# Kernel tuning notes

Hardware: AMD Instinct MI355X
Metric: run time of the kernel (lower is better)

Reference implementation:

```python
import jax, jax.numpy as jnp
import numpy as np

TOTAL = 262144
FEAT = 512
NSEG = 1024


def setup_inputs() -> dict:
    key = jax.random.key(0)
    k1, k2 = jax.random.split(key)
    batch = jax.random.normal(k1, (TOTAL, FEAT), dtype=jnp.float32)
    segment_ids = jnp.sort(jax.random.randint(k2, (TOTAL,), 0, NSEG)).astype(jnp.int32)
    return {"batch": batch, "segment_ids": segment_ids, "num_segments": NSEG}


def reference(batch, segment_ids, num_segments):
    # mode='mean', keep_shape=True: per-segment mean, broadcast back to rows.
    seg_sum = jax.ops.segment_sum(batch, segment_ids, num_segments=num_segments)
    counts = jax.ops.segment_sum(
        jnp.ones((batch.shape[0],), dtype=batch.dtype), segment_ids,
        num_segments=num_segments)
    means = seg_sum / jnp.maximum(counts, 1.0)[:, None]  # [NSEG, FEAT]
    out = jnp.take(means, segment_ids, axis=0)           # keep_shape expand
    return out
```

## Files before the change

### kernel.cpp

```cpp
#include <hip/hip_runtime.h>

#define FEAT 512
#define F4   128
#define NSEG 1024
#define CHUNK 256

typedef float f4_t __attribute__((ext_vector_type(4)));

__global__ void bounds_zero_kernel(const int* __restrict__ seg,
                                   int* __restrict__ starts,
                                   float* __restrict__ sums, int total) {
    int i = blockIdx.x * blockDim.x + threadIdx.x;
    if (sums != nullptr && i < NSEG * FEAT / 2) {
        ((float2*)sums)[i] = make_float2(0.f, 0.f);
    }
    if (i >= total) return;
    int cur = seg[i];
    int prev = (i == 0) ? -1 : seg[i - 1];
    for (int s = prev + 1; s <= cur; ++s) starts[s] = i;
    if (i == total - 1) {
        for (int s = cur + 1; s <= NSEG; ++s) starts[s] = total;
    }
}

__global__ __launch_bounds__(512) void chunk_sum_kernel(
        const float* __restrict__ batch,
        const int* __restrict__ seg,
        const int* __restrict__ starts,
        float* __restrict__ sums, int total) {
    const int tid  = threadIdx.x;
    const int lane = tid & (F4 - 1);
    const int rg   = tid >> 7;
    const int r0   = blockIdx.x * CHUNK;
    if (r0 >= total) return;
    const int r1   = min(r0 + CHUNK, total);

    const int s0 = seg[r0];
    const int s1 = seg[r1 - 1];

    const f4_t* b4 = (const f4_t*)batch;
    __shared__ f4_t red[4][F4];

    for (int s = s0; s <= s1; ++s) {
        const int a = max(starts[s], r0);
        const int b = min(starts[s + 1], r1);
        if (a >= b) continue;

        f4_t a0 = (f4_t)(0.f);
        f4_t a1 = (f4_t)(0.f);
        int r = a + rg;
        for (; r + 28 < b; r += 32) {
            const f4_t* p = b4 + (size_t)r * F4 + lane;
            f4_t v0 = __builtin_nontemporal_load(p + 0 * 4 * F4);
            f4_t v1 = __builtin_nontemporal_load(p + 1 * 4 * F4);
            f4_t v2 = __builtin_nontemporal_load(p + 2 * 4 * F4);
            f4_t v3 = __builtin_nontemporal_load(p + 3 * 4 * F4);
            f4_t v4 = __builtin_nontemporal_load(p + 4 * 4 * F4);
            f4_t v5 = __builtin_nontemporal_load(p + 5 * 4 * F4);
            f4_t v6 = __builtin_nontemporal_load(p + 6 * 4 * F4);
            f4_t v7 = __builtin_nontemporal_load(p + 7 * 4 * F4);
            a0 += v0; a1 += v1;
            a0 += v2; a1 += v3;
            a0 += v4; a1 += v5;
            a0 += v6; a1 += v7;
        }
        for (; r < b; r += 4) {
            a0 += __builtin_nontemporal_load(b4 + (size_t)r * F4 + lane);
        }
        a0 += a1;

        red[rg][lane] = a0;
        __syncthreads();
        if (rg == 0) {
            f4_t t = red[0][lane] + red[1][lane] + red[2][lane] + red[3][lane];
            float* dst = sums + (size_t)s * FEAT + lane * 4;
            atomicAdd(dst + 0, t.x);
            atomicAdd(dst + 1, t.y);
            atomicAdd(dst + 2, t.z);
            atomicAdd(dst + 3, t.w);
        }
        __syncthreads();
    }
}

__global__ __launch_bounds__(256) void broadcast_chunk_kernel(
        const int* __restrict__ seg,
        const int* __restrict__ starts,
        const float* __restrict__ sums,
        float* __restrict__ out, int total) {
    const int tid  = threadIdx.x;
    const int lane = tid & (F4 - 1);
    const int rg   = tid >> 7;
    const int r0   = blockIdx.x * CHUNK;
    if (r0 >= total) return;
    const int r1   = min(r0 + CHUNK, total);

    const int s0 = seg[r0];
    const int s1 = seg[r1 - 1];

    const f4_t* m4 = (const f4_t*)sums;
    f4_t* o4 = (f4_t*)out;

    for (int s = s0; s <= s1; ++s) {
        const int sa = starts[s];
        const int sb = starts[s + 1];
        const int a = max(sa, r0);
        const int b = min(sb, r1);
        if (a >= b) continue;
        const int count = sb - sa;
        const float inv = 1.0f / (float)(count > 0 ? count : 1);
        const f4_t mean = m4[(size_t)s * F4 + lane] * inv;
        int r = a + rg;
        for (; r + 14 < b; r += 16) {
            f4_t* q = o4 + (size_t)r * F4 + lane;
            __builtin_nontemporal_store(mean, q + 0 * 2 * F4);
            __builtin_nontemporal_store(mean, q + 1 * 2 * F4);
            __builtin_nontemporal_store(mean, q + 2 * 2 * F4);
            __builtin_nontemporal_store(mean, q + 3 * 2 * F4);
            __builtin_nontemporal_store(mean, q + 4 * 2 * F4);
            __builtin_nontemporal_store(mean, q + 5 * 2 * F4);
            __builtin_nontemporal_store(mean, q + 6 * 2 * F4);
            __builtin_nontemporal_store(mean, q + 7 * 2 * F4);
        }
        for (; r < b; r += 2) {
            __builtin_nontemporal_store(mean, o4 + (size_t)r * F4 + lane);
        }
    }
}

__global__ __launch_bounds__(512) void seg_mean_fused_kernel(
        const float* __restrict__ batch,
        const int* __restrict__ starts,
        float* __restrict__ out) {
    const int s      = blockIdx.x;
    const int tid    = threadIdx.x;
    const int lane_f = tid & (F4 - 1);
    const int rgrp   = tid >> 7;

    const int start = starts[s];
    const int end   = starts[s + 1];
    const int count = end - start;

    const f4_t* b4 = (const f4_t*)batch;
    f4_t a0 = (f4_t)(0.f);
    f4_t a1 = (f4_t)(0.f);

    int r = start + rgrp;
    for (; r + 28 < end; r += 32) {
        const f4_t* p = b4 + (size_t)r * F4 + lane_f;
        f4_t v0 = __builtin_nontemporal_load(p + 0 * 4 * F4);
        f4_t v1 = __builtin_nontemporal_load(p + 1 * 4 * F4);
        f4_t v2 = __builtin_nontemporal_load(p + 2 * 4 * F4);
        f4_t v3 = __builtin_nontemporal_load(p + 3 * 4 * F4);
        f4_t v4 = __builtin_nontemporal_load(p + 4 * 4 * F4);
        f4_t v5 = __builtin_nontemporal_load(p + 5 * 4 * F4);
        f4_t v6 = __builtin_nontemporal_load(p + 6 * 4 * F4);
        f4_t v7 = __builtin_nontemporal_load(p + 7 * 4 * F4);
        a0 += v0; a1 += v1;
        a0 += v2; a1 += v3;
        a0 += v4; a1 += v5;
        a0 += v6; a1 += v7;
    }
    for (; r < end; r += 4) {
        a0 += __builtin_nontemporal_load(b4 + (size_t)r * F4 + lane_f);
    }
    a0 += a1;

    __shared__ f4_t red[4][F4];
    red[rgrp][lane_f] = a0;
    __syncthreads();

    if (rgrp == 0) {
        f4_t p0 = red[0][lane_f];
        f4_t p1 = red[1][lane_f];
        f4_t p2 = red[2][lane_f];
        f4_t p3 = red[3][lane_f];
        const float inv = 1.0f / (float)(count > 0 ? count : 1);
        red[0][lane_f] = (p0 + p1 + p2 + p3) * inv;
    }
    __syncthreads();

    const f4_t mean = red[0][lane_f];
    f4_t* o4 = (f4_t*)out;

    r = start + rgrp;
    for (; r + 28 < end; r += 32) {
        f4_t* q = o4 + (size_t)r * F4 + lane_f;
        __builtin_nontemporal_store(mean, q + 0 * 4 * F4);
        __builtin_nontemporal_store(mean, q + 1 * 4 * F4);
        __builtin_nontemporal_store(mean, q + 2 * 4 * F4);
        __builtin_nontemporal_store(mean, q + 3 * 4 * F4);
        __builtin_nontemporal_store(mean, q + 4 * 4 * F4);
        __builtin_nontemporal_store(mean, q + 5 * 4 * F4);
        __builtin_nontemporal_store(mean, q + 6 * 4 * F4);
        __builtin_nontemporal_store(mean, q + 7 * 4 * F4);
    }
    for (; r < end; r += 4) {
        __builtin_nontemporal_store(mean, o4 + (size_t)r * F4 + lane_f);
    }
}

extern "C" void kernel_launch(void* const* d_in, const int* in_sizes, int n_in,
                              void* d_out, int out_size, void* d_ws, size_t ws_size,
                              hipStream_t stream) {
    const float* batch = (const float*)d_in[0];
    const int*   seg   = (const int*)d_in[1];
    float*       out   = (float*)d_out;
    const int total    = in_sizes[1];

    const size_t sums_bytes = (size_t)NSEG * FEAT * sizeof(float);
    const size_t need       = sums_bytes + (NSEG + 1) * sizeof(int);

    const int nblk256 = (total + 255) / 256;

    if (ws_size >= need) {
        float* sums   = (float*)d_ws;
        int*   starts = (int*)((char*)d_ws + sums_bytes);

        bounds_zero_kernel<<<nblk256, 256, 0, stream>>>(seg, starts, sums, total);
        const int nchunks = (total + CHUNK - 1) / CHUNK;
        chunk_sum_kernel<<<nchunks, 512, 0, stream>>>(batch, seg, starts, sums, total);
        broadcast_chunk_kernel<<<nchunks, 256, 0, stream>>>(seg, starts, sums, out, total);
    } else {
        int* starts = (int*)d_ws;
        bounds_zero_kernel<<<nblk256, 256, 0, stream>>>(seg, starts, nullptr, total);
        seg_mean_fused_kernel<<<NSEG, 512, 0, stream>>>(batch, starts, out);
    }
}
```

Before: 197.6 us.

## Fuse chunk sum and broadcast for segments contained within one chunk

Chunks grow to 1024 rows with 1024-thread blocks. A segment that lies entirely inside one chunk now has its mean computed and written straight back to the output in the same kernel, without a global atomic round trip. Segments that span chunks still accumulate into the workspace with atomics, and a per-segment kernel broadcasts only those. This cuts a separate launch and the full broadcast pass over most rows, at the cost of larger blocks, fewer of them (256), and extra barriers.

```diff
diff --git a/kernel.cpp b/kernel.cpp
--- a/kernel.cpp
+++ b/kernel.cpp
@@ -3,7 +3,8 @@
 #define FEAT 512
 #define F4   128
 #define NSEG 1024
-#define CHUNK 256
+#define CHUNK 1024
+#define NRG   8
 
 typedef float f4_t __attribute__((ext_vector_type(4)));
 
@@ -23,70 +24,11 @@
     }
 }
 
-__global__ __launch_bounds__(512) void chunk_sum_kernel(
+__global__ __launch_bounds__(1024) void fused_sum_bcast_kernel(
         const float* __restrict__ batch,
         const int* __restrict__ seg,
         const int* __restrict__ starts,
-        float* __restrict__ sums, int total) {
-    const int tid  = threadIdx.x;
-    const int lane = tid & (F4 - 1);
-    const int rg   = tid >> 7;
-    const int r0   = blockIdx.x * CHUNK;
-    if (r0 >= total) return;
-    const int r1   = min(r0 + CHUNK, total);
-
-    const int s0 = seg[r0];
-    const int s1 = seg[r1 - 1];
-
-    const f4_t* b4 = (const f4_t*)batch;
-    __shared__ f4_t red[4][F4];
-
-    for (int s = s0; s <= s1; ++s) {
-        const int a = max(starts[s], r0);
-        const int b = min(starts[s + 1], r1);
-        if (a >= b) continue;
-
-        f4_t a0 = (f4_t)(0.f);
-        f4_t a1 = (f4_t)(0.f);
-        int r = a + rg;
-        for (; r + 28 < b; r += 32) {
-            const f4_t* p = b4 + (size_t)r * F4 + lane;
-            f4_t v0 = __builtin_nontemporal_load(p + 0 * 4 * F4);
-            f4_t v1 = __builtin_nontemporal_load(p + 1 * 4 * F4);
-            f4_t v2 = __builtin_nontemporal_load(p + 2 * 4 * F4);
-            f4_t v3 = __builtin_nontemporal_load(p + 3 * 4 * F4);
-            f4_t v4 = __builtin_nontemporal_load(p + 4 * 4 * F4);
-            f4_t v5 = __builtin_nontemporal_load(p + 5 * 4 * F4);
-            f4_t v6 = __builtin_nontemporal_load(p + 6 * 4 * F4);
-            f4_t v7 = __builtin_nontemporal_load(p + 7 * 4 * F4);
-            a0 += v0; a1 += v1;
-            a0 += v2; a1 += v3;
-            a0 += v4; a1 += v5;
-            a0 += v6; a1 += v7;
-        }
-        for (; r < b; r += 4) {
-            a0 += __builtin_nontemporal_load(b4 + (size_t)r * F4 + lane);
-        }
-        a0 += a1;
-
-        red[rg][lane] = a0;
-        __syncthreads();
-        if (rg == 0) {
-            f4_t t = red[0][lane] + red[1][lane] + red[2][lane] + red[3][lane];
-            float* dst = sums + (size_t)s * FEAT + lane * 4;
-            atomicAdd(dst + 0, t.x);
-            atomicAdd(dst + 1, t.y);
-            atomicAdd(dst + 2, t.z);
-            atomicAdd(dst + 3, t.w);
-        }
-        __syncthreads();
-    }
-}
-
-__global__ __launch_bounds__(256) void broadcast_chunk_kernel(
-        const int* __restrict__ seg,
-        const int* __restrict__ starts,
-        const float* __restrict__ sums,
+        float* __restrict__ sums,
         float* __restrict__ out, int total) {
     const int tid  = threadIdx.x;
     const int lane = tid & (F4 - 1);
@@ -98,8 +40,9 @@
     const int s0 = seg[r0];
     const int s1 = seg[r1 - 1];
 
-    const f4_t* m4 = (const f4_t*)sums;
+    const f4_t* b4 = (const f4_t*)batch;
     f4_t* o4 = (f4_t*)out;
+    __shared__ f4_t red[NRG][F4];
 
     for (int s = s0; s <= s1; ++s) {
         const int sa = starts[s];
@@ -107,24 +50,99 @@
         const int a = max(sa, r0);
         const int b = min(sb, r1);
         if (a >= b) continue;
-        const int count = sb - sa;
-        const float inv = 1.0f / (float)(count > 0 ? count : 1);
-        const f4_t mean = m4[(size_t)s * F4 + lane] * inv;
+        const bool interior = (sa >= r0) && (sb <= r1);
+
+        f4_t a0 = (f4_t)(0.f);
+        f4_t a1 = (f4_t)(0.f);
         int r = a + rg;
-        for (; r + 14 < b; r += 16) {
-            f4_t* q = o4 + (size_t)r * F4 + lane;
-            __builtin_nontemporal_store(mean, q + 0 * 2 * F4);
-            __builtin_nontemporal_store(mean, q + 1 * 2 * F4);
-            __builtin_nontemporal_store(mean, q + 2 * 2 * F4);
-            __builtin_nontemporal_store(mean, q + 3 * 2 * F4);
-            __builtin_nontemporal_store(mean, q + 4 * 2 * F4);
-            __builtin_nontemporal_store(mean, q + 5 * 2 * F4);
-            __builtin_nontemporal_store(mean, q + 6 * 2 * F4);
-            __builtin_nontemporal_store(mean, q + 7 * 2 * F4);
-        }
-        for (; r < b; r += 2) {
-            __builtin_nontemporal_store(mean, o4 + (size_t)r * F4 + lane);
-        }
+        for (; r + 7 * NRG < b; r += 8 * NRG) {
+            const f4_t* p = b4 + (size_t)r * F4 + lane;
+            f4_t v0 = __builtin_nontemporal_load(p + 0 * NRG * F4);
+            f4_t v1 = __builtin_nontemporal_load(p + 1 * NRG * F4);
+            f4_t v2 = __builtin_nontemporal_load(p + 2 * NRG * F4);
+            f4_t v3 = __builtin_nontemporal_load(p + 3 * NRG * F4);
+            f4_t v4 = __builtin_nontemporal_load(p + 4 * NRG * F4);
+            f4_t v5 = __builtin_nontemporal_load(p + 5 * NRG * F4);
+            f4_t v6 = __builtin_nontemporal_load(p + 6 * NRG * F4);
+            f4_t v7 = __builtin_nontemporal_load(p + 7 * NRG * F4);
+            a0 += v0; a1 += v1;
+            a0 += v2; a1 += v3;
+            a0 += v4; a1 += v5;
+            a0 += v6; a1 += v7;
+        }
+        for (; r < b; r += NRG) {
+            a0 += __builtin_nontemporal_load(b4 + (size_t)r * F4 + lane);
+        }
+        a0 += a1;
+
+        red[rg][lane] = a0;
+        __syncthreads();
+        if (rg == 0) {
+            f4_t t = red[0][lane];
+            #pragma unroll
+            for (int g = 1; g < NRG; ++g) t += red[g][lane];
+            if (interior) {
+                const float inv = 1.0f / (float)(sb - sa);
+                red[0][lane] = t * inv;
+            } else {
+                float* dst = sums + (size_t)s * FEAT + lane * 4;
+                atomicAdd(dst + 0, t.x);
+                atomicAdd(dst + 1, t.y);
+                atomicAdd(dst + 2, t.z);
+                atomicAdd(dst + 3, t.w);
+            }
+        }
+        __syncthreads();
+        if (interior) {
+            const f4_t mean = red[0][lane];
+            __syncthreads();
+            int r2 = a + rg;
+            for (; r2 + 7 * NRG < b; r2 += 8 * NRG) {
+                f4_t* q = o4 + (size_t)r2 * F4 + lane;
+                __builtin_nontemporal_store(mean, q + 0 * NRG * F4);
+                __builtin_nontemporal_store(mean, q + 1 * NRG * F4);
+                __builtin_nontemporal_store(mean, q + 2 * NRG * F4);
+                __builtin_nontemporal_store(mean, q + 3 * NRG * F4);
+                __builtin_nontemporal_store(mean, q + 4 * NRG * F4);
+                __builtin_nontemporal_store(mean, q + 5 * NRG * F4);
+                __builtin_nontemporal_store(mean, q + 6 * NRG * F4);
+                __builtin_nontemporal_store(mean, q + 7 * NRG * F4);
+            }
+            for (; r2 < b; r2 += NRG) {
+                __builtin_nontemporal_store(mean, o4 + (size_t)r2 * F4 + lane);
+            }
+        }
+    }
+}
+
+__global__ __launch_bounds__(256) void boundary_bcast_kernel(
+        const int* __restrict__ starts,
+        const float* __restrict__ sums,
+        float* __restrict__ out, int total) {
+    const int s  = blockIdx.x;
+    const int sa = starts[s];
+    const int sb = starts[s + 1];
+    if (sa >= sb) return;
+    if (sa / CHUNK == (sb - 1) / CHUNK) return;
+    const int lane = threadIdx.x & (F4 - 1);
+    const int rg   = threadIdx.x >> 7;
+    const float inv = 1.0f / (float)(sb - sa);
+    const f4_t mean = ((const f4_t*)sums)[(size_t)s * F4 + lane] * inv;
+    f4_t* o4 = (f4_t*)out;
+    int r = sa + rg;
+    for (; r + 14 < sb; r += 16) {
+        f4_t* q = o4 + (size_t)r * F4 + lane;
+        __builtin_nontemporal_store(mean, q + 0 * 2 * F4);
+        __builtin_nontemporal_store(mean, q + 1 * 2 * F4);
+        __builtin_nontemporal_store(mean, q + 2 * 2 * F4);
+        __builtin_nontemporal_store(mean, q + 3 * 2 * F4);
+        __builtin_nontemporal_store(mean, q + 4 * 2 * F4);
+        __builtin_nontemporal_store(mean, q + 5 * 2 * F4);
+        __builtin_nontemporal_store(mean, q + 6 * 2 * F4);
+        __builtin_nontemporal_store(mean, q + 7 * 2 * F4);
+    }
+    for (; r < sb; r += 2) {
+        __builtin_nontemporal_store(mean, o4 + (size_t)r * F4 + lane);
     }
 }
 
@@ -219,8 +237,8 @@
 
         bounds_zero_kernel<<<nblk256, 256, 0, stream>>>(seg, starts, sums, total);
         const int nchunks = (total + CHUNK - 1) / CHUNK;
-        chunk_sum_kernel<<<nchunks, 512, 0, stream>>>(batch, seg, starts, sums, total);
-        broadcast_chunk_kernel<<<nchunks, 256, 0, stream>>>(seg, starts, sums, out, total);
+        fused_sum_bcast_kernel<<<nchunks, 1024, 0, stream>>>(batch, seg, starts, sums, out, total);
+        boundary_bcast_kernel<<<NSEG, 256, 0, stream>>>(starts, sums, out, total);
     } else {
         int* starts = (int*)d_ws;
         bounds_zero_kernel<<<nblk256, 256, 0, stream>>>(seg, starts, nullptr, total);
```

After: 217.8 us. +10.2%, slower.

## Split sum/broadcast into halves so broadcasting the first half overlaps summing the second

Applied to the files above, without the earlier changes.

Segment summation now runs in two halves. A first kernel sums the first half of the rows. A middle kernel then writes out the means of segments that end inside the first half, while its other blocks sum the second half. A final kernel broadcasts the remaining segments. Overlapping the stores with the loads is meant to keep both read and write bandwidth busy, at the cost of an extra launch and extra loops over segment ranges. The broadcast also moves to 512 threads, and the count guard is dropped because every non-empty segment has count > 0.

```diff
diff --git a/kernel.cpp b/kernel.cpp
--- a/kernel.cpp
+++ b/kernel.cpp
@@ -23,29 +23,16 @@
     }
 }
 
-__global__ __launch_bounds__(512) void chunk_sum_kernel(
-        const float* __restrict__ batch,
-        const int* __restrict__ seg,
-        const int* __restrict__ starts,
-        float* __restrict__ sums, int total) {
-    const int tid  = threadIdx.x;
-    const int lane = tid & (F4 - 1);
-    const int rg   = tid >> 7;
-    const int r0   = blockIdx.x * CHUNK;
-    if (r0 >= total) return;
-    const int r1   = min(r0 + CHUNK, total);
-
+__device__ __forceinline__ void sum_chunk_body(
+        const f4_t* __restrict__ b4, const int* __restrict__ seg,
+        const int* __restrict__ starts, float* __restrict__ sums,
+        f4_t (*red)[F4], int r0, int r1, int lane, int rg) {
     const int s0 = seg[r0];
     const int s1 = seg[r1 - 1];
-
-    const f4_t* b4 = (const f4_t*)batch;
-    __shared__ f4_t red[4][F4];
-
     for (int s = s0; s <= s1; ++s) {
         const int a = max(starts[s], r0);
         const int b = min(starts[s + 1], r1);
         if (a >= b) continue;
-
         f4_t a0 = (f4_t)(0.f);
         f4_t a1 = (f4_t)(0.f);
         int r = a + rg;
@@ -83,49 +70,84 @@
     }
 }
 
-__global__ __launch_bounds__(256) void broadcast_chunk_kernel(
-        const int* __restrict__ seg,
-        const int* __restrict__ starts,
-        const float* __restrict__ sums,
-        float* __restrict__ out, int total) {
-    const int tid  = threadIdx.x;
-    const int lane = tid & (F4 - 1);
-    const int rg   = tid >> 7;
-    const int r0   = blockIdx.x * CHUNK;
-    if (r0 >= total) return;
-    const int r1   = min(r0 + CHUNK, total);
-
+template <bool LE>
+__device__ __forceinline__ void bcast_chunk_body(
+        const int* __restrict__ seg, const int* __restrict__ starts,
+        const float* __restrict__ sums, f4_t* __restrict__ o4,
+        int r0, int r1, int limit, int lane, int rg, int nrg) {
     const int s0 = seg[r0];
     const int s1 = seg[r1 - 1];
-
     const f4_t* m4 = (const f4_t*)sums;
-    f4_t* o4 = (f4_t*)out;
-
     for (int s = s0; s <= s1; ++s) {
         const int sa = starts[s];
         const int sb = starts[s + 1];
+        if (LE ? (sb > limit) : (sb <= limit)) continue;
         const int a = max(sa, r0);
         const int b = min(sb, r1);
         if (a >= b) continue;
-        const int count = sb - sa;
-        const float inv = 1.0f / (float)(count > 0 ? count : 1);
+        const float inv = 1.0f / (float)(sb - sa);
         const f4_t mean = m4[(size_t)s * F4 + lane] * inv;
         int r = a + rg;
-        for (; r + 14 < b; r += 16) {
+        for (; r + 7 * nrg < b; r += 8 * nrg) {
             f4_t* q = o4 + (size_t)r * F4 + lane;
-            __builtin_nontemporal_store(mean, q + 0 * 2 * F4);
-            __builtin_nontemporal_store(mean, q + 1 * 2 * F4);
-            __builtin_nontemporal_store(mean, q + 2 * 2 * F4);
-            __builtin_nontemporal_store(mean, q + 3 * 2 * F4);
-            __builtin_nontemporal_store(mean, q + 4 * 2 * F4);
-            __builtin_nontemporal_store(mean, q + 5 * 2 * F4);
-            __builtin_nontemporal_store(mean, q + 6 * 2 * F4);
-            __builtin_nontemporal_store(mean, q + 7 * 2 * F4);
-        }
-        for (; r < b; r += 2) {
+            __builtin_nontemporal_store(mean, q + 0 * nrg * F4);
+            __builtin_nontemporal_store(mean, q + 1 * nrg * F4);
+            __builtin_nontemporal_store(mean, q + 2 * nrg * F4);
+            __builtin_nontemporal_store(mean, q + 3 * nrg * F4);
+            __builtin_nontemporal_store(mean, q + 4 * nrg * F4);
+            __builtin_nontemporal_store(mean, q + 5 * nrg * F4);
+            __builtin_nontemporal_store(mean, q + 6 * nrg * F4);
+            __builtin_nontemporal_store(mean, q + 7 * nrg * F4);
+        }
+        for (; r < b; r += nrg) {
             __builtin_nontemporal_store(mean, o4 + (size_t)r * F4 + lane);
         }
     }
+}
+
+__global__ __launch_bounds__(512) void sum_a_kernel(
+        const float* __restrict__ batch, const int* __restrict__ seg,
+        const int* __restrict__ starts, float* __restrict__ sums, int total) {
+    __shared__ f4_t red[4][F4];
+    const int r0 = blockIdx.x * CHUNK;
+    if (r0 >= total) return;
+    const int r1 = min(r0 + CHUNK, total);
+    sum_chunk_body((const f4_t*)batch, seg, starts, sums, red, r0, r1,
+                   threadIdx.x & (F4 - 1), threadIdx.x >> 7);
+}
+
+__global__ __launch_bounds__(512) void mid_kernel(
+        const float* __restrict__ batch, const int* __restrict__ seg,
+        const int* __restrict__ starts, float* __restrict__ sums,
+        float* __restrict__ out, int total, int halfc, int half_rows) {
+    __shared__ f4_t red[4][F4];
+    const int lane = threadIdx.x & (F4 - 1);
+    const int rg   = threadIdx.x >> 7;
+    const int bid  = blockIdx.x;
+    if (bid < halfc) {
+        const int r0 = bid * CHUNK;
+        if (r0 >= total) return;
+        const int r1 = min(r0 + CHUNK, total);
+        bcast_chunk_body<true>(seg, starts, sums, (f4_t*)out,
+                               r0, r1, half_rows, lane, rg, 4);
+    } else {
+        const int r0 = bid * CHUNK;
+        if (r0 >= total) return;
+        const int r1 = min(r0 + CHUNK, total);
+        sum_chunk_body((const f4_t*)batch, seg, starts, sums, red, r0, r1, lane, rg);
+    }
+}
+
+__global__ __launch_bounds__(512) void bcast_b_kernel(
+        const int* __restrict__ seg, const int* __restrict__ starts,
+        const float* __restrict__ sums, float* __restrict__ out,
+        int total, int half_rows) {
+    const int r0 = blockIdx.x * CHUNK;
+    if (r0 >= total) return;
+    const int r1 = min(r0 + CHUNK, total);
+    bcast_chunk_body<false>(seg, starts, sums, (f4_t*)out,
+                            r0, r1, half_rows, threadIdx.x & (F4 - 1),
+                            threadIdx.x >> 7, 4);
 }
 
 __global__ __launch_bounds__(512) void seg_mean_fused_kernel(
@@ -217,10 +239,16 @@
         float* sums   = (float*)d_ws;
         int*   starts = (int*)((char*)d_ws + sums_bytes);
 
+        const int nchunks   = (total + CHUNK - 1) / CHUNK;
+        const int halfc     = nchunks / 2;
+        const int half_rows = halfc * CHUNK;
+
         bounds_zero_kernel<<<nblk256, 256, 0, stream>>>(seg, starts, sums, total);
-        const int nchunks = (total + CHUNK - 1) / CHUNK;
-        chunk_sum_kernel<<<nchunks, 512, 0, stream>>>(batch, seg, starts, sums, total);
-        broadcast_chunk_kernel<<<nchunks, 256, 0, stream>>>(seg, starts, sums, out, total);
+        sum_a_kernel<<<halfc, 512, 0, stream>>>(batch, seg, starts, sums, half_rows);
+        mid_kernel<<<nchunks, 512, 0, stream>>>(batch, seg, starts, sums, out,
+                                                total, halfc, half_rows);
+        bcast_b_kernel<<<nchunks, 512, 0, stream>>>(seg, starts, sums, out,
+                                                    total, half_rows);
     } else {
         int* starts = (int*)d_ws;
         bounds_zero_kernel<<<nblk256, 256, 0, stream>>>(seg, starts, nullptr, total);
```

Result: slower. 203.3 us (+2.9%).
